# Kernel optimization log

Hardware: AMD Instinct MI355X
Metric: run time of the kernel (lower is better)

## Reference

```python
import jax, jax.numpy as jnp
import numpy as np

H = 4096      # hidden_size
NH = 32       # num_heads
QR = 1536     # q_lora_rank
KVR = 512     # kv_lora_rank
RD = 64       # qk_rope_head_dim
ND = 128      # qk_nope_head_dim
VD = 128      # v_head_dim
QK = RD + ND  # qk_head_dim
EPS = 1e-6
THETA = 10000.0
B, S = 2, 1024


def rmsnorm(x, w):
    # torch: x / (||x|| * d^-0.5 + eps) * w
    norm = jnp.sqrt(jnp.sum(x * x, axis=-1, keepdims=True)) * (x.shape[-1] ** -0.5)
    return x / (norm + EPS) * w


def rope_cos_sin(seq_len):
    inv_freq = 1.0 / (THETA ** (jnp.arange(0, RD, 2, dtype=jnp.float32) / RD))
    t = jnp.arange(seq_len, dtype=jnp.float32)
    freqs = jnp.outer(t, inv_freq)              # [S, RD/2]
    emb = jnp.concatenate([freqs, freqs], -1)   # [S, RD]
    return jnp.cos(emb), jnpp_cos_sin_dummy() if False else jnp.sin(emb)


def rotate_half(x):
    x1, x2 = jnp.split(x, 2, axis=-1)
    return jnp.concatenate([-x2, x1], axis=-1)


def setup_inputs() -> dict:
    key = jax.random.key(0)
    ks = jax.random.split(key, 8)
    sc = 0.02
    return {
        "hidden_states": jax.random.normal(ks[0], (B, S, H), jnp.float32),
        "w_qa": jax.random.normal(ks[1], (H, QR), jnp.float32) * sc,
        "g_qa": jnp.ones((QR,), jnp.float32),
        "w_qb": jax.random.normal(ks[2], (QR, NH * QK), jnp.float32) * sc,
        "w_kva": jax.random.normal(ks[3], (H, KVR + RD), jnp.float32) * sc,
        "g_kva": jnp.ones((KVR,), jnp.float32),
        "w_kvb": jax.random.normal(ks[4], (KVR, NH * (ND + VD)), jnp.float32) * sc,
        "w_o": jax.random.normal(ks[5], (NH * VD, H), jnp.float32) * sc,
    }


def reference(hidden_states, w_qa, g_qa, w_qb, w_kva, g_kva, w_kvb, w_o):
    b, s, _ = hidden_states.shape
    # Q path: LoRA down -> RMSNorm -> LoRA up
    q_c = rmsnorm(hidden_states @ w_qa, g_qa)                       # [b,s,QR]
    q = (q_c @ w_qb).reshape(b, s, NH, QK).transpose(0, 2, 1, 3)    # [b,NH,s,QK]
    q_nope, q_rope = q[..., :ND], q[..., ND:]
    # KV path: joint down-proj, split compressed kv and rope key
    kv = hidden_states @ w_kva                                      # [b,s,KVR+RD]
    k_c, k_rope = kv[..., :KVR], kv[..., KVR:]
    k_c = rmsnorm(k_c, g_kva)
    kst = (k_c @ w_kvb).reshape(b, s, NH, ND + VD).transpose(0, 2, 1, 3)
    k_nope, v = kst[..., :ND], kst[..., ND:]                        # [b,NH,s,ND],[b,NH,s,VD]
    # partial RoPE on the rope slice only
    inv_freq = 1.0 / (THETA ** (jnp.arange(0, RD, 2, dtype=jnp.float32) / RD))
    freqs = jnp.outer(jnp.arange(s, dtype=jnp.float32), inv_freq)
    emb = jnp.concatenate([freqs, freqs], -1)                       # [s,RD]
    cos = jnp.cos(emb)[None, None]                                  # [1,1,s,RD]
    sin = jnp.sin(emb)[None, None]
    k_rope = k_rope[:, None]                                        # [b,1,s,RD]
    q_rope = q_rope * cos + rotate_half(q_rope) * sin
    k_rope = k_rope * cos + rotate_half(k_rope) * sin
    k_rope = jnp.broadcast_to(k_rope, (b, NH, s, RD))
    query = jnp.concatenate([q_nope, q_rope], -1)                   # [b,NH,s,QK]
    key_s = jnp.concatenate([k_nope, k_rope], -1)
    scaling = QK ** -0.5
    scores = jnp.einsum("bhqd,bhkd->bhqk", query, key_s) * scaling  # [b,NH,s,s]
    attn = jax.nn.softmax(scores, axis=-1)
    out = jnp.einsum("bhqk,bhkd->bhqd", attn, v)                    # [b,NH,s,VD]
    out = out.transpose(0, 2, 1, 3).reshape(b, s, NH * VD)
    return out @ w_o                                                # [b,s,H]
```

## Files before the change

kernel.cpp:

```cpp
#include <hip/hip_runtime.h>
#include <hip/hip_bf16.h>
#include <stdint.h>

typedef float f32x4_t __attribute__((ext_vector_type(4)));
typedef short s16x8_t __attribute__((ext_vector_type(8)));

#define LDS_AS __attribute__((address_space(3)))
#define GLB_AS __attribute__((address_space(1)))

__device__ __forceinline__ void gload16(void* lds, const void* g) {
    __builtin_amdgcn_global_load_lds((const GLB_AS uint32_t*)g,
                                     (LDS_AS uint32_t*)lds, 16, 0, 0);
}

__device__ __forceinline__ uint32_t pack_bf16(float lo, float hi) {
    union { __hip_bfloat16 h; uint16_t u; } a, b;
    a.h = __float2bfloat16(lo); b.h = __float2bfloat16(hi);
    return (uint32_t)a.u | ((uint32_t)b.u << 16);
}

__global__ __launch_bounds__(256) void rope_table_kernel(float* __restrict__ cos_t,
                                                         float* __restrict__ sin_t) {
    int idx = blockIdx.x * 256 + threadIdx.x;
    int s = idx >> 6, j = idx & 63;
    float invf = powf(10000.0f, -((float)((j & 31) * 2)) / 64.0f);
    float a = (float)s * invf;
    cos_t[idx] = cosf(a);
    sin_t[idx] = sinf(a);
}

__global__ __launch_bounds__(256) void f32_to_bf16_kernel(const float* __restrict__ in,
                                                          __hip_bfloat16* __restrict__ out, int n4) {
    int i = blockIdx.x * 256 + threadIdx.x;
    if (i >= n4) return;
    float4 v = reinterpret_cast<const float4*>(in)[i];
    struct __align__(8) BF4 { __hip_bfloat16 a, b, c, d; } r;
    r.a = __float2bfloat16(v.x); r.b = __float2bfloat16(v.y);
    r.c = __float2bfloat16(v.z); r.d = __float2bfloat16(v.w);
    reinterpret_cast<BF4*>(out)[i] = r;
}

__global__ __launch_bounds__(256) void transpose_convert(const float* __restrict__ W,
                                                         __hip_bfloat16* __restrict__ WT,
                                                         int K, int N, int Npad, float scale) {
    __shared__ float tile[32][132];
    int k0 = blockIdx.y * 32, n0 = blockIdx.x * 128;
    int tx = threadIdx.x & 31, ty = threadIdx.x >> 5;
#pragma unroll
    for (int i = 0; i < 4; i++) {
        int ky = i * 8 + ty;
        int n = n0 + tx * 4;
        float4 v;
        if (n + 3 < N) {
            v = *(const float4*)&W[(size_t)(k0 + ky) * N + n];
        } else {
            float t0 = (n + 0 < N) ? W[(size_t)(k0 + ky) * N + n + 0] : 0.f;
            float t1 = (n + 1 < N) ? W[(size_t)(k0 + ky) * N + n + 1] : 0.f;
            float t2 = (n + 2 < N) ? W[(size_t)(k0 + ky) * N + n + 2] : 0.f;
            float t3 = (n + 3 < N) ? W[(size_t)(k0 + ky) * N + n + 3] : 0.f;
            v = make_float4(t0, t1, t2, t3);
        }
        *(float4*)&tile[ky][tx * 4] = v;
    }
    __syncthreads();
    int ny = threadIdx.x & 127, kh = threadIdx.x >> 7;
#pragma unroll
    for (int oct = 0; oct < 2; oct++) {
        int kb = kh * 16 + oct * 8;
        union { short s[8]; s16x8_t v; } pk;
#pragma unroll
        for (int e = 0; e < 8; e++) {
            union { __hip_bfloat16 h; short s; } cv;
            cv.h = __float2bfloat16(tile[kb + e][ny] * scale);
            pk.s[e] = cv.s;
        }
        *(s16x8_t*)&WT[(size_t)(n0 + ny) * K + k0 + kb] = pk.v;
    }
}

__global__ __launch_bounds__(256) void rmsnorm_kernel(const float* __restrict__ in,
                                                      const float* __restrict__ g,
                                                      __hip_bfloat16* __restrict__ out,
                                                      int cols, int in_stride) {
    int row = blockIdx.x;
    const float* x = in + (size_t)row * in_stride;
    float ss = 0.f;
    for (int c = threadIdx.x; c < cols; c += 256) { float v = x[c]; ss += v * v; }
#pragma unroll
    for (int off = 32; off > 0; off >>= 1) ss += __shfl_xor(ss, off);
    __shared__ float red[4];
    if ((threadIdx.x & 63) == 0) red[threadIdx.x >> 6] = ss;
    __syncthreads();
    float tot = red[0] + red[1] + red[2] + red[3];
    float rms = sqrtf(tot / (float)cols);
    float inv = 1.0f / (rms + 1e-6f);
    for (int c = threadIdx.x; c < cols; c += 256)
        out[(size_t)row * cols + c] = __float2bfloat16(x[c] * inv * g[c]);
}

__global__ __launch_bounds__(256) void rope_k_kernel(const float* __restrict__ kv,
                                                     const float* __restrict__ cos_t,
                                                     const float* __restrict__ sin_t,
                                                     __hip_bfloat16* __restrict__ k_rope) {
    int idx = blockIdx.x * 256 + threadIdx.x;
    int tok = idx >> 5, j = idx & 31;
    int s = tok & 1023;
    const float* x = kv + (size_t)tok * 640 + 512;
    float x1 = x[j], x2 = x[j + 32];
    float co = cos_t[s * 64 + j], si = sin_t[s * 64 + j];
    __hip_bfloat16* o = k_rope + (size_t)tok * 64;
    o[j]      = __float2bfloat16(x1 * co - x2 * si);
    o[j + 32] = __float2bfloat16(x2 * co + x1 * si);
}

__global__ __launch_bounds__(256) void rope_q_kernel(__hip_bfloat16* __restrict__ q,
                                                     const float* __restrict__ cos_t,
                                                     const float* __restrict__ sin_t) {
    int tok = blockIdx.x;
    int s = tok & 1023;
    __hip_bfloat16* row = q + (size_t)tok * 6144;
#pragma unroll
    for (int it = 0; it < 4; it++) {
        int i = it * 256 + threadIdx.x;
        int h = i >> 5, j = i & 31;
        int c = h * 192 + 128 + j;
        float x1 = __bfloat162float(row[c]), x2 = __bfloat162float(row[c + 32]);
        float co = cos_t[s * 64 + j], si = sin_t[s * 64 + j];
        row[c]      = __float2bfloat16(x1 * co - x2 * si);
        row[c + 32] = __float2bfloat16(x2 * co + x1 * si);
    }
}

__global__ __launch_bounds__(256) void transpose_v_kernel(const __hip_bfloat16* __restrict__ kst,
                                                          __hip_bfloat16* __restrict__ V_T) {
    __shared__ __hip_bfloat16 t[64][136];
    int bid = blockIdx.x;
    int st = bid & 15, bh = bid >> 4;
    int h = bh & 31, b = bh >> 5;
    int s0 = st * 64;
#pragma unroll
    for (int i = 0; i < 4; i++) {
        int c = i * 256 + threadIdx.x;
        int r = c >> 4, oct = c & 15;
        *(s16x8_t*)&t[r][oct * 8] =
            *(const s16x8_t*)&kst[(size_t)(b * 1024 + s0 + r) * 8192 + h * 256 + 128 + oct * 8];
    }
    __syncthreads();
#pragma unroll
    for (int i = 0; i < 4; i++) {
        int c = i * 256 + threadIdx.x;
        int vd = c >> 3, oct = c & 7;
        s16x8_t pk;
#pragma unroll
        for (int e = 0; e < 8; e++) pk[e] = *(const short*)&t[oct * 8 + e][vd];
        *(s16x8_t*)&V_T[((size_t)bh * 128 + vd) * 1024 + s0 + oct * 8] = pk;
    }
}

template <int MODE>
__global__ __launch_bounds__(256, 3) void gemm_bt_128(const __hip_bfloat16* __restrict__ A,
                                                      const __hip_bfloat16* __restrict__ BT,
                                                      void* __restrict__ Cout, void* __restrict__ C1,
                                                      int M, int N, int K, int N0, int N1) {
    __shared__ __hip_bfloat16 As[128 * 64];
    __shared__ __hip_bfloat16 Bs[128 * 64];
    const int tid = threadIdx.x;
    const int l = tid & 63, w = tid >> 6;
    const int wr = w >> 1, wc = w & 1;
    const int m0 = blockIdx.y * 128, n0 = blockIdx.x * 128;
    const int lrow = l & 15, lkg = l >> 4;

    f32x4_t acc[4][4];
#pragma unroll
    for (int i = 0; i < 4; i++)
#pragma unroll
        for (int j = 0; j < 4; j++) acc[i][j] = (f32x4_t){0.f, 0.f, 0.f, 0.f};

    for (int k0 = 0; k0 < K; k0 += 64) {
        __syncthreads();
#pragma unroll
        for (int i = 0; i < 4; i++) {
            int s = i * 256 + tid;
            int row = s >> 3, po = s & 7;
            int lo = po ^ (row & 7);
            gload16(&As[s * 8], &A[(size_t)(m0 + row) * K + k0 + lo * 8]);
            gload16(&Bs[s * 8], &BT[(size_t)(n0 + row) * K + k0 + lo * 8]);
        }
        __syncthreads();
#pragma unroll
        for (int ks = 0; ks < 2; ks++) {
            s16x8_t a[4], b[4];
#pragma unroll
            for (int m = 0; m < 4; m++) {
                int row = wr * 64 + m * 16 + lrow;
                int oct = (ks * 4 + lkg) ^ (row & 7);
                a[m] = *(const s16x8_t*)&As[row * 64 + oct * 8];
            }
#pragma unroll
            for (int n = 0; n < 4; n++) {
                int row = wc * 64 + n * 16 + lrow;
                int oct = (ks * 4 + lkg) ^ (row & 7);
                b[n] = *(const s16x8_t*)&Bs[row * 64 + oct * 8];
            }
#pragma unroll
            for (int m = 0; m < 4; m++)
#pragma unroll
                for (int n = 0; n < 4; n++)
                    acc[m][n] = __builtin_amdgcn_mfma_f32_16x16x32_bf16(a[m], b[n], acc[m][n], 0, 0, 0);
        }
    }
#pragma unroll
    for (int m = 0; m < 4; m++) {
        int row = m0 + wr * 64 + m * 16 + lkg * 4;
#pragma unroll
        for (int n = 0; n < 4; n++) {
            int col = n0 + wc * 64 + n * 16 + lrow;
#pragma unroll
            for (int r = 0; r < 4; r++) {
                float v = acc[m][n][r];
                if (MODE == 1) {
                    ((__hip_bfloat16*)Cout)[(size_t)(row + r) * N + col] = __float2bfloat16(v);
                } else if (MODE == 0) {
                    ((float*)Cout)[(size_t)(row + r) * N + col] = v;
                } else {
                    if (col < N0) ((float*)Cout)[(size_t)(row + r) * N0 + col] = v;
                    else          ((float*)C1)[(size_t)(row + r) * N1 + (col - N0)] = v;
                }
            }
        }
    }
}

__global__ __launch_bounds__(256, 3) void attn8_kernel(const __hip_bfloat16* __restrict__ q,
                                                       const __hip_bfloat16* __restrict__ kst,
                                                       const __hip_bfloat16* __restrict__ k_rope,
                                                       const __hip_bfloat16* __restrict__ V_T,
                                                       __hip_bfloat16* __restrict__ attn_out) {
    __shared__ __align__(16) __hip_bfloat16 Ks[2][64 * 192];

    int i = blockIdx.x;
    int bh = (i & 7) * 8 + ((i >> 3) & 7);
    int qt = i >> 6;
    int h = bh & 31, b = bh >> 5;
    int q0 = qt * 64;
    int tid = threadIdx.x, l = tid & 63, w = tid >> 6;
    int lrow = l & 15, lkg = l >> 4;

    s16x8_t qa[6];
    {
        size_t qbase = (size_t)(b * 1024 + q0 + w * 16 + lrow) * 6144 + h * 192;
#pragma unroll
        for (int f = 0; f < 6; f++)
            qa[f] = *(const s16x8_t*)&q[qbase + f * 32 + lkg * 8];
    }
    f32x4_t acc_o[8];
#pragma unroll
    for (int n = 0; n < 8; n++) acc_o[n] = (f32x4_t){0.f, 0.f, 0.f, 0.f};
    float m_run = -1e30f, l_run = 0.f;

    size_t krow_base = (size_t)(b * 1024) * 8192 + h * 256;
    size_t rrow_base = (size_t)(b * 1024) * 64;
    const __hip_bfloat16* vbase = V_T + (size_t)bh * 128 * 1024 + (size_t)lrow * 1024 + lkg * 8;

    auto stage_k = [&](int kv0, int buf) {
#pragma unroll
        for (int it = 0; it < 6; it++) {
            int s = it * 256 + tid;
            int row = s / 24, po = s - row * 24;
            int lo = po ^ (row & 7);
            const __hip_bfloat16* src = (lo < 16)
                ? &kst[krow_base + (size_t)(kv0 + row) * 8192 + lo * 8]
                : &k_rope[rrow_base + (size_t)(kv0 + row) * 64 + (lo - 16) * 8];
            gload16(&Ks[buf][s * 8], src);
        }
    };

    stage_k(0, 0);
    asm volatile("s_waitcnt vmcnt(0)" ::: "memory");
    __syncthreads();

    const int src0 = lrow + ((lkg & 1) << 5);
    const int src1 = src0 + 16;
    const bool hiC = (lkg >> 1) != 0;

    int cur = 0;
    for (int kt = 0; kt < 16; kt++) {
        int kv0 = kt * 64;

        if (kt < 15) stage_k(kv0 + 64, cur ^ 1);

        f32x4_t sc[4];
#pragma unroll
        for (int c = 0; c < 4; c++) sc[c] = (f32x4_t){0.f, 0.f, 0.f, 0.f};
        __builtin_amdgcn_s_setprio(1);
#pragma unroll
        for (int c = 0; c < 4; c++) {
            int row = c * 16 + lrow;
#pragma unroll
            for (int f = 0; f < 6; f++) {
                int po = ((f * 4 + lkg) ^ (lrow & 7)) * 8;
                s16x8_t kb = *(const s16x8_t*)&Ks[cur][row * 192 + po];
                sc[c] = __builtin_amdgcn_mfma_f32_16x16x32_bf16(kb, qa[f], sc[c], 0, 0, 0);
            }
        }
        __builtin_amdgcn_s_setprio(0);

        s16x8_t vb0[8];
#pragma unroll
        for (int n = 0; n < 8; n++)
            vb0[n] = *(const s16x8_t*)&vbase[(size_t)(n * 16) * 1024 + kv0];
        __builtin_amdgcn_sched_barrier(0);

        float mx = sc[0][0];
#pragma unroll
        for (int c = 0; c < 4; c++)
#pragma unroll
            for (int r = 0; r < 4; r++) mx = fmaxf(mx, sc[c][r]);
        mx = fmaxf(mx, __shfl_xor(mx, 16));
        mx = fmaxf(mx, __shfl_xor(mx, 32));
        if (!__all(mx - m_run <= 8.0f)) {
            float mn = fmaxf(m_run, mx);
            float al = __expf(m_run - mn);
            m_run = mn;
            l_run *= al;
#pragma unroll
            for (int n = 0; n < 8; n++) acc_o[n] *= al;
        }
        uint32_t u[4][2];
        float sum = 0.f;
#pragma unroll
        for (int c = 0; c < 4; c++) {
            float p0 = __expf(sc[c][0] - m_run), p1 = __expf(sc[c][1] - m_run);
            float p2 = __expf(sc[c][2] - m_run), p3 = __expf(sc[c][3] - m_run);
            sum += (p0 + p1) + (p2 + p3);
            u[c][0] = pack_bf16(p0, p1);
            u[c][1] = pack_bf16(p2, p3);
        }
        sum += __shfl_xor(sum, 16);
        sum += __shfl_xor(sum, 32);
        l_run += sum;

        {
            uint32_t a0 = __shfl((int)u[0][0], src0), b0 = __shfl((int)u[1][0], src0);
            uint32_t a1 = __shfl((int)u[0][1], src0), b1 = __shfl((int)u[1][1], src0);
            uint32_t a2 = __shfl((int)u[0][0], src1), b2 = __shfl((int)u[1][0], src1);
            uint32_t a3 = __shfl((int)u[0][1], src1), b3 = __shfl((int)u[1][1], src1);
            union { uint32_t wd[4]; s16x8_t v; } pb;
            pb.wd[0] = hiC ? b0 : a0;
            pb.wd[1] = hiC ? b1 : a1;
            pb.wd[2] = hiC ? b2 : a2;
            pb.wd[3] = hiC ? b3 : a3;
            __builtin_amdgcn_s_setprio(1);
#pragma unroll
            for (int n = 0; n < 8; n++)
                acc_o[n] = __builtin_amdgcn_mfma_f32_16x16x32_bf16(vb0[n], pb.v, acc_o[n], 0, 0, 0);
            __builtin_amdgcn_s_setprio(0);
        }
        s16x8_t vb1[8];
#pragma unroll
        for (int n = 0; n < 8; n++)
            vb1[n] = *(const s16x8_t*)&vbase[(size_t)(n * 16) * 1024 + kv0 + 32];
        {
            uint32_t a0 = __shfl((int)u[2][0], src0), b0 = __shfl((int)u[3][0], src0);
            uint32_t a1 = __shfl((int)u[2][1], src0), b1 = __shfl((int)u[3][1], src0);
            uint32_t a2 = __shfl((int)u[2][0], src1), b2 = __shfl((int)u[3][0], src1);
            uint32_t a3 = __shfl((int)u[2][1], src1), b3 = __shfl((int)u[3][1], src1);
            union { uint32_t wd[4]; s16x8_t v; } pb;
            pb.wd[0] = hiC ? b0 : a0;
            pb.wd[1] = hiC ? b1 : a1;
            pb.wd[2] = hiC ? b2 : a2;
            pb.wd[3] = hiC ? b3 : a3;
            __builtin_amdgcn_s_setprio(1);
#pragma unroll
            for (int n = 0; n < 8; n++)
                acc_o[n] = __builtin_amdgcn_mfma_f32_16x16x32_bf16(vb1[n], pb.v, acc_o[n], 0, 0, 0);
            __builtin_amdgcn_s_setprio(0);
        }

        asm volatile("s_waitcnt vmcnt(0)" ::: "memory");
        __syncthreads();
        cur ^= 1;
    }

    float inv = 1.0f / l_run;
    __hip_bfloat16* Ob = &Ks[0][0] + (size_t)w * (16 * 136);
#pragma unroll
    for (int n = 0; n < 8; n++) {
        uint32_t lo = pack_bf16(acc_o[n][0] * inv, acc_o[n][1] * inv);
        uint32_t hi = pack_bf16(acc_o[n][2] * inv, acc_o[n][3] * inv);
        uint32_t* dst = (uint32_t*)&Ob[lrow * 136 + n * 16 + lkg * 4];
        dst[0] = lo;
        dst[1] = hi;
    }
    asm volatile("s_waitcnt lgkmcnt(0)" ::: "memory");
    __builtin_amdgcn_sched_barrier(0);
#pragma unroll
    for (int it = 0; it < 4; it++) {
        int tr = it * 4 + lkg;
        s16x8_t ov = *(const s16x8_t*)&Ob[tr * 136 + lrow * 8];
        *(s16x8_t*)&attn_out[(size_t)(b * 1024 + q0 + w * 16 + tr) * 4096 + h * 128 + lrow * 8] = ov;
    }
}

extern "C" void kernel_launch(void* const* d_in, const int* in_sizes, int n_in,
                              void* d_out, int out_size, void* d_ws, size_t ws_size,
                              hipStream_t stream) {
    const float* hidden = (const float*)d_in[0];
    const float* w_qa   = (const float*)d_in[1];
    const float* g_qa   = (const float*)d_in[2];
    const float* w_qb   = (const float*)d_in[3];
    const float* w_kva  = (const float*)d_in[4];
    const float* g_kva  = (const float*)d_in[5];
    const float* w_kvb  = (const float*)d_in[6];
    const float* w_o    = (const float*)d_in[7];
    float* out = (float*)d_out;

    char* base = (char*)d_ws;
    size_t off = 0;
    auto alloc = [&](size_t bytes) -> void* {
        off = (off + 255) & ~(size_t)255;
        void* p = base + off;
        off += bytes;
        return p;
    };
    float* cos_t = (float*)alloc(1024 * 64 * 4);
    float* sin_t = (float*)alloc(1024 * 64 * 4);
    __hip_bfloat16* hid_b  = (__hip_bfloat16*)alloc(2048ull * 4096 * 2);
    __hip_bfloat16* wqaT   = (__hip_bfloat16*)alloc(1536ull * 4096 * 2);
    __hip_bfloat16* wkvaT  = (__hip_bfloat16*)alloc(640ull * 4096 * 2);
    __hip_bfloat16* wqbT   = (__hip_bfloat16*)alloc(6144ull * 1536 * 2);
    __hip_bfloat16* wkvbT  = (__hip_bfloat16*)alloc(8192ull * 512 * 2);
    __hip_bfloat16* woT    = (__hip_bfloat16*)alloc(4096ull * 4096 * 2);
    float* q_a             = (float*)alloc(2048ull * 1536 * 4);
    __hip_bfloat16* q_c    = (__hip_bfloat16*)alloc(2048ull * 1536 * 2);
    __hip_bfloat16* q_buf  = (__hip_bfloat16*)alloc(2048ull * 6144 * 2);
    float* kv              = (float*)alloc(2048ull * 640 * 4);
    __hip_bfloat16* k_c    = (__hip_bfloat16*)alloc(2048ull * 512 * 2);
    __hip_bfloat16* k_rope = (__hip_bfloat16*)alloc(2048ull * 64 * 2);
    __hip_bfloat16* kst    = (__hip_bfloat16*)alloc(2048ull * 8192 * 2);
    __hip_bfloat16* V_T      = hid_b;
    __hip_bfloat16* attn_out = wqbT;

    const float qscale = 0.07216878364870323f;

    rope_table_kernel<<<256, 256, 0, stream>>>(cos_t, sin_t);
    f32_to_bf16_kernel<<<8192, 256, 0, stream>>>(hidden, hid_b, 2048 * 4096 / 4);
    transpose_convert<<<dim3(1536 / 128, 4096 / 32), 256, 0, stream>>>(w_qa, wqaT, 4096, 1536, 1536, 1.0f);
    transpose_convert<<<dim3(640 / 128, 4096 / 32), 256, 0, stream>>>(w_kva, wkvaT, 4096, 576, 640, 1.0f);
    transpose_convert<<<dim3(6144 / 128, 1536 / 32), 256, 0, stream>>>(w_qb, wqbT, 1536, 6144, 6144, qscale);
    transpose_convert<<<dim3(8192 / 128, 512 / 32), 256, 0, stream>>>(w_kvb, wkvbT, 512, 8192, 8192, 1.0f);
    transpose_convert<<<dim3(4096 / 128, 4096 / 32), 256, 0, stream>>>(w_o, woT, 4096, 4096, 4096, 1.0f);

    gemm_bt_128<2><<<dim3(17, 16), 256, 0, stream>>>(hid_b, wqaT, q_a, kv, 2048, 2176, 4096, 1536, 640);
    rmsnorm_kernel<<<2048, 256, 0, stream>>>(q_a, g_qa, q_c, 1536, 1536);
    rmsnorm_kernel<<<2048, 256, 0, stream>>>(kv, g_kva, k_c, 512, 640);
    rope_k_kernel<<<2048 * 32 / 256, 256, 0, stream>>>(kv, cos_t, sin_t, k_rope);
    gemm_bt_128<1><<<dim3(6144 / 128, 16), 256, 0, stream>>>(q_c, wqbT, q_buf, nullptr, 2048, 6144, 1536, 0, 0);
    rope_q_kernel<<<2048, 256, 0, stream>>>(q_buf, cos_t, sin_t);
    gemm_bt_128<1><<<dim3(8192 / 128, 16), 256, 0, stream>>>(k_c, wkvbT, kst, nullptr, 2048, 8192, 512, 0, 0);
    transpose_v_kernel<<<1024, 256, 0, stream>>>(kst, V_T);
    attn8_kernel<<<1024, 256, 0, stream>>>(q_buf, kst, k_rope, V_T, attn_out);
    gemm_bt_128<0><<<dim3(4096 / 128, 16), 256, 0, stream>>>(attn_out, woT, out, nullptr, 2048, 4096, 4096, 0, 0);
}
```

Before: 462.1 us.

## Split-K the fused down-projection GEMM and fuse q RoPE into up-projection epilogue

```diff
diff --git a/kernel.cpp b/kernel.cpp
--- a/kernel.cpp
+++ b/kernel.cpp
@@ -78,14 +78,16 @@
     }
 }
 
-__global__ __launch_bounds__(256) void rmsnorm_kernel(const float* __restrict__ in,
-                                                      const float* __restrict__ g,
-                                                      __hip_bfloat16* __restrict__ out,
-                                                      int cols, int in_stride) {
+__global__ __launch_bounds__(256) void rmsnorm2_kernel(const float* __restrict__ in0,
+                                                       const float* __restrict__ in1,
+                                                       const float* __restrict__ g,
+                                                       __hip_bfloat16* __restrict__ out,
+                                                       int cols, int in_stride) {
     int row = blockIdx.x;
-    const float* x = in + (size_t)row * in_stride;
+    const float* x0 = in0 + (size_t)row * in_stride;
+    const float* x1 = in1 + (size_t)row * in_stride;
     float ss = 0.f;
-    for (int c = threadIdx.x; c < cols; c += 256) { float v = x[c]; ss += v * v; }
+    for (int c = threadIdx.x; c < cols; c += 256) { float v = x0[c] + x1[c]; ss += v * v; }
 #pragma unroll
     for (int off = 32; off > 0; off >>= 1) ss += __shfl_xor(ss, off);
     __shared__ float red[4];
@@ -95,40 +97,24 @@
     float rms = sqrtf(tot / (float)cols);
     float inv = 1.0f / (rms + 1e-6f);
     for (int c = threadIdx.x; c < cols; c += 256)
-        out[(size_t)row * cols + c] = __float2bfloat16(x[c] * inv * g[c]);
-}
-
-__global__ __launch_bounds__(256) void rope_k_kernel(const float* __restrict__ kv,
-                                                     const float* __restrict__ cos_t,
-                                                     const float* __restrict__ sin_t,
-                                                     __hip_bfloat16* __restrict__ k_rope) {
+        out[(size_t)row * cols + c] = __float2bfloat16((x0[c] + x1[c]) * inv * g[c]);
+}
+
+__global__ __launch_bounds__(256) void rope_k2_kernel(const float* __restrict__ kv0,
+                                                      const float* __restrict__ kv1,
+                                                      const float* __restrict__ cos_t,
+                                                      const float* __restrict__ sin_t,
+                                                      __hip_bfloat16* __restrict__ k_rope) {
     int idx = blockIdx.x * 256 + threadIdx.x;
     int tok = idx >> 5, j = idx & 31;
     int s = tok & 1023;
-    const float* x = kv + (size_t)tok * 640 + 512;
-    float x1 = x[j], x2 = x[j + 32];
+    size_t base = (size_t)tok * 640 + 512;
+    float x1 = kv0[base + j] + kv1[base + j];
+    float x2 = kv0[base + j + 32] + kv1[base + j + 32];
     float co = cos_t[s * 64 + j], si = sin_t[s * 64 + j];
     __hip_bfloat16* o = k_rope + (size_t)tok * 64;
     o[j]      = __float2bfloat16(x1 * co - x2 * si);
     o[j + 32] = __float2bfloat16(x2 * co + x1 * si);
-}
-
-__global__ __launch_bounds__(256) void rope_q_kernel(__hip_bfloat16* __restrict__ q,
-                                                     const float* __restrict__ cos_t,
-                                                     const float* __restrict__ sin_t) {
-    int tok = blockIdx.x;
-    int s = tok & 1023;
-    __hip_bfloat16* row = q + (size_t)tok * 6144;
-#pragma unroll
-    for (int it = 0; it < 4; it++) {
-        int i = it * 256 + threadIdx.x;
-        int h = i >> 5, j = i & 31;
-        int c = h * 192 + 128 + j;
-        float x1 = __bfloat162float(row[c]), x2 = __bfloat162float(row[c + 32]);
-        float co = cos_t[s * 64 + j], si = sin_t[s * 64 + j];
-        row[c]      = __float2bfloat16(x1 * co - x2 * si);
-        row[c + 32] = __float2bfloat16(x2 * co + x1 * si);
-    }
 }
 
 __global__ __launch_bounds__(256) void transpose_v_kernel(const __hip_bfloat16* __restrict__ kst,
@@ -161,7 +147,10 @@
 __global__ __launch_bounds__(256, 3) void gemm_bt_128(const __hip_bfloat16* __restrict__ A,
                                                       const __hip_bfloat16* __restrict__ BT,
                                                       void* __restrict__ Cout, void* __restrict__ C1,
-                                                      int M, int N, int K, int N0, int N1) {
+                                                      void* __restrict__ Cout2, void* __restrict__ C12,
+                                                      int M, int N, int K, int Kstride, int N0, int N1,
+                                                      const float* __restrict__ cos_t,
+                                                      const float* __restrict__ sin_t) {
     __shared__ __hip_bfloat16 As[128 * 64];
     __shared__ __hip_bfloat16 Bs[128 * 64];
     const int tid = threadIdx.x;
@@ -169,6 +158,8 @@
     const int wr = w >> 1, wc = w & 1;
     const int m0 = blockIdx.y * 128, n0 = blockIdx.x * 128;
     const int lrow = l & 15, lkg = l >> 4;
+    const int part = (MODE == 2) ? blockIdx.z : 0;
+    const int kbase = part * K;
 
     f32x4_t acc[4][4];
 #pragma unroll
@@ -183,8 +174,8 @@
             int s = i * 256 + tid;
             int row = s >> 3, po = s & 7;
             int lo = po ^ (row & 7);
-            gload16(&As[s * 8], &A[(size_t)(m0 + row) * K + k0 + lo * 8]);
-            gload16(&Bs[s * 8], &BT[(size_t)(n0 + row) * K + k0 + lo * 8]);
+            gload16(&As[s * 8], &A[(size_t)(m0 + row) * Kstride + kbase + k0 + lo * 8]);
+            gload16(&Bs[s * 8], &BT[(size_t)(n0 + row) * Kstride + kbase + k0 + lo * 8]);
         }
         __syncthreads();
 #pragma unroll
@@ -209,6 +200,7 @@
                     acc[m][n] = __builtin_amdgcn_mfma_f32_16x16x32_bf16(a[m], b[n], acc[m][n], 0, 0, 0);
         }
     }
+    const bool ropeblk = (MODE == 3) && ((((n0 + wc * 64) >> 6) % 3) == 2);
 #pragma unroll
     for (int m = 0; m < 4; m++) {
         int row = m0 + wr * 64 + m * 16 + lkg * 4;
@@ -218,13 +210,22 @@
 #pragma unroll
             for (int r = 0; r < 4; r++) {
                 float v = acc[m][n][r];
-                if (MODE == 1) {
+                if (MODE == 3 && ropeblk) {
+                    int s = (row + r) & 1023;
+                    int j = ((n & 1) << 4) + lrow;
+                    float co = cos_t[s * 64 + j], si = sin_t[s * 64 + j];
+                    v = (n < 2) ? acc[m][n][r] * co - acc[m][n + 2][r] * si
+                                : acc[m][n][r] * co + acc[m][n - 2][r] * si;
+                }
+                if (MODE == 1 || MODE == 3) {
                     ((__hip_bfloat16*)Cout)[(size_t)(row + r) * N + col] = __float2bfloat16(v);
                 } else if (MODE == 0) {
                     ((float*)Cout)[(size_t)(row + r) * N + col] = v;
                 } else {
-                    if (col < N0) ((float*)Cout)[(size_t)(row + r) * N0 + col] = v;
-                    else          ((float*)C1)[(size_t)(row + r) * N1 + (col - N0)] = v;
+                    float* c0 = (float*)(part ? Cout2 : Cout);
+                    float* c1 = (float*)(part ? C12 : C1);
+                    if (col < N0) c0[(size_t)(row + r) * N0 + col] = v;
+                    else          c1[(size_t)(row + r) * N1 + (col - N0)] = v;
                 }
             }
         }
@@ -440,6 +441,8 @@
     __hip_bfloat16* kst    = (__hip_bfloat16*)alloc(2048ull * 8192 * 2);
     __hip_bfloat16* V_T      = hid_b;
     __hip_bfloat16* attn_out = wqbT;
+    float* q_a1 = (float*)q_buf;
+    float* kv1  = (float*)((char*)q_buf + 2048ull * 1536 * 4);
 
     const float qscale = 0.07216878364870323f;
 
@@ -451,14 +454,18 @@
     transpose_convert<<<dim3(8192 / 128, 512 / 32), 256, 0, stream>>>(w_kvb, wkvbT, 512, 8192, 8192, 1.0f);
     transpose_convert<<<dim3(4096 / 128, 4096 / 32), 256, 0, stream>>>(w_o, woT, 4096, 4096, 4096, 1.0f);
 
-    gemm_bt_128<2><<<dim3(17, 16), 256, 0, stream>>>(hid_b, wqaT, q_a, kv, 2048, 2176, 4096, 1536, 640);
-    rmsnorm_kernel<<<2048, 256, 0, stream>>>(q_a, g_qa, q_c, 1536, 1536);
-    rmsnorm_kernel<<<2048, 256, 0, stream>>>(kv, g_kva, k_c, 512, 640);
-    rope_k_kernel<<<2048 * 32 / 256, 256, 0, stream>>>(kv, cos_t, sin_t, k_rope);
-    gemm_bt_128<1><<<dim3(6144 / 128, 16), 256, 0, stream>>>(q_c, wqbT, q_buf, nullptr, 2048, 6144, 1536, 0, 0);
-    rope_q_kernel<<<2048, 256, 0, stream>>>(q_buf, cos_t, sin_t);
-    gemm_bt_128<1><<<dim3(8192 / 128, 16), 256, 0, stream>>>(k_c, wkvbT, kst, nullptr, 2048, 8192, 512, 0, 0);
+    gemm_bt_128<2><<<dim3(17, 16, 2), 256, 0, stream>>>(hid_b, wqaT, q_a, kv, q_a1, kv1,
+                                                        2048, 2176, 2048, 4096, 1536, 640,
+                                                        nullptr, nullptr);
+    rmsnorm2_kernel<<<2048, 256, 0, stream>>>(q_a, q_a1, g_qa, q_c, 1536, 1536);
+    rmsnorm2_kernel<<<2048, 256, 0, stream>>>(kv, kv1, g_kva, k_c, 512, 640);
+    rope_k2_kernel<<<2048 * 32 / 256, 256, 0, stream>>>(kv, kv1, cos_t, sin_t, k_rope);
+    gemm_bt_128<3><<<dim3(6144 / 128, 16), 256, 0, stream>>>(q_c, wqbT, q_buf, nullptr, nullptr, nullptr,
+                                                             2048, 6144, 1536, 1536, 0, 0, cos_t, sin_t);
+    gemm_bt_128<1><<<dim3(8192 / 128, 16), 256, 0, stream>>>(k_c, wkvbT, kst, nullptr, nullptr, nullptr,
+                                                             2048, 8192, 512, 512, 0, 0, nullptr, nullptr);
     transpose_v_kernel<<<1024, 256, 0, stream>>>(kst, V_T);
     attn8_kernel<<<1024, 256, 0, stream>>>(q_buf, kst, k_rope, V_T, attn_out);
-    gemm_bt_128<0><<<dim3(4096 / 128, 16), 256, 0, stream>>>(attn_out, woT, out, nullptr, 2048, 4096, 4096, 0, 0);
-}
+    gemm_bt_128<0><<<dim3(4096 / 128, 16), 256, 0, stream>>>(attn_out, woT, out, nullptr, nullptr, nullptr,
+                                                             2048, 4096, 4096, 4096, 0, 0, nullptr, nullptr);
+}
```

Result: no change. 456.2 us (-1.3%).
